# Kernel tuning notes

Measured on AMD Instinct MI355X. Metric: run time of the kernel, lower is better.

## Reference

```python
import jax, jax.numpy as jnp
import numpy as np

SIGMA_DATA = 16.0
ALPHA_BOND = 1.0
ALPHA_DNA = 5.0
ALPHA_RNA = 5.0
ALPHA_LIGAND = 10.0
B, N_TOK, APT = 2, 256, 8
N_ATOM = N_TOK * APT
EPS = 1e-12  # inside sqrt to keep grads finite on the zero diagonal


def _pdist(x):
    # x: [*, A, 3] -> [*, A, A]
    d = x[..., :, None, :] - x[..., None, :, :]
    return jnp.sqrt(jnp.sum(d * d, axis=-1) + EPS)


def _atom_onehot(token_mask, num_atoms_per_token, n_atom):
    # [*, A, T]: atom l belongs to token j iff cum[j-1] <= l < cum[j]
    cum = jnp.cumsum(num_atoms_per_token, axis=-1)
    start = cum - num_atoms_per_token
    l = jnp.arange(n_atom)
    oh = (l[:, None] >= start[..., None, :]) & (l[:, None] < cum[..., None, :])
    return oh.astype(jnp.float32) * token_mask[..., None, :]


def _tok_to_atom(onehot, feat):
    return jnp.einsum('...lj,...j->...l', onehot, feat)


def _weighted_rigid_align(x, x_gt, w, mask):
    # AF3 Algorithm 28 (Kabsch); output is detached in the original.
    denom = jnp.sum(mask, -1, keepdims=True)                      # [*,1]
    w_mean = jnp.sum(w * mask, -1, keepdims=True) / denom         # [*,1]
    wm = (w * mask)[..., None]                                    # [*,A,1]
    mu = (jnp.sum(x * wm, -2) / denom) / w_mean                   # [*,3]
    mu_gt = (jnp.sum(x_gt * wm, -2) / denom) / w_mean
    xc = x - mu[..., None, :]
    xgc = x_gt - mu_gt[..., None, :]
    H = jnp.einsum('...ai,...aj->...ij', xgc * wm, xc)            # [*,3,3]
    U, _, Vh = jnp.linalg.svd(H)
    det = jnp.linalg.det(U @ Vh)
    s = jnp.concatenate([jnp.ones(det.shape + (2,), H.dtype), jnp.sign(det)[..., None]], -1)
    R = U @ (Vh * s[..., :, None])                                # U @ diag(1,1,sign) @ Vh
    return jax.lax.stop_gradient(xc @ jnp.swapaxes(R, -1, -2) + mu_gt[..., None, :])


def _diffusion_loss(x, gt, gt_mask, is_p, is_d, is_r, is_l, tb, tm, npt, t):
    A = x.shape[-2]
    oh = _atom_onehot(tm, npt, A)                                 # [*,A,T]
    dx = _pdist(x)
    dx_gt = _pdist(gt)
    pair_mask = gt_mask[..., :, None] * gt_mask[..., None, :]

    # ---- bond loss (Eq. 5) ----
    is_poly = is_p + is_d + is_r
    bm_tok = tb * (is_poly[..., None, :] * is_l[..., None])       # [*,T,T]
    bm = jnp.einsum('...ij,...li->...lj', bm_tok, oh)
    bm = jnp.einsum('...lj,...mj->...lm', bm, oh)                 # [*,A,A]
    m = bm * pair_mask
    l_bond = jnp.sum((dx - dx_gt) ** 2 * m, (-1, -2)) / jnp.sum(m, (-1, -2))

    # ---- smooth LDDT (Alg. 27) ----
    d = jnp.abs(dx_gt - dx)
    e = 0.25 * (jax.nn.sigmoid(0.5 - d) + jax.nn.sigmoid(1.0 - d)
                + jax.nn.sigmoid(2.0 - d) + jax.nn.sigmoid(4.0 - d))
    is_nuc = _tok_to_atom(oh, is_d + is_r)                        # [*,A]
    c = ((dx_gt < 30).astype(x.dtype) * is_nuc[..., None]
         + (dx_gt < 15).astype(x.dtype) * (1.0 - is_nuc[..., None]))
    m2 = (1.0 - jnp.eye(A, dtype=x.dtype)) * pair_mask
    msum = jnp.sum(m2, (-1, -2))
    ce_mean = jnp.sum(c * e * m2, (-1, -2)) / msum
    c_mean = jnp.sum(c * m2, (-1, -2)) / msum
    l_lddt = 1.0 - ce_mean / c_mean

    # ---- weighted MSE (Eq. 3), gt aligned onto x ----
    w_tok = 1.0 + is_d * ALPHA_DNA + is_r * ALPHA_RNA + is_l * ALPHA_LIGAND
    w_atom = _tok_to_atom(oh, w_tok)                              # [*,A]
    sg = jax.lax.stop_gradient
    gt_al = _weighted_rigid_align(sg(gt), sg(x), sg(w_atom), sg(gt_mask))
    l_mse = (1.0 / 3.0) * jnp.sum(jnp.sum((x - gt_al) ** 2, -1) * w_atom * gt_mask, -1) \
            / jnp.sum(gt_mask, -1)

    w_t = (t ** 2 + SIGMA_DATA ** 2) / (t + SIGMA_DATA) ** 2
    return jnp.mean(w_t * (l_mse + ALPHA_BOND * l_bond) + l_lddt)


def setup_inputs() -> dict:
    key = jax.random.key(0)
    k = jax.random.split(key, 9)
    x = jax.random.normal(k[0], (B, N_ATOM, 3), jnp.float32) * 10.0
    gt = x + jax.random.normal(k[1], (B, N_ATOM, 3), jnp.float32)
    return {
        'x': x,
        'gt_atom_positions': gt,
        'gt_atom_mask': jnp.ones((B, N_ATOM), jnp.float32),
        'is_protein': jax.random.uniform(k[2], (B, N_TOK), jnp.float32),
        'is_dna': jax.random.uniform(k[3], (B, N_TOK), jnp.float32),
        'is_rna': jax.random.uniform(k[4], (B, N_TOK), jnp.float32),
        'is_ligand': jax.random.uniform(k[5], (B, N_TOK), jnp.float32),
        'token_bonds': jax.random.uniform(k[6], (B, N_TOK, N_TOK), jnp.float32),
        'token_mask': jnp.ones((B, N_TOK), jnp.float32),
        'num_atoms_per_token': jnp.full((B, N_TOK), APT, jnp.int32),
        't': jax.random.uniform(k[7], (B,), jnp.float32) * 10.0 + 0.1,
    }


def reference(x, gt_atom_positions, gt_atom_mask, is_protein, is_dna, is_rna,
              is_ligand, token_bonds, token_mask, num_atoms_per_token, t):
    return _diffusion_loss(x, gt_atom_positions, gt_atom_mask, is_protein, is_dna,
                           is_rna, is_ligand, token_bonds, token_mask,
                           num_atoms_per_token, t)
```

## Files before the change

kernel.cpp:

```cpp
#include <hip/hip_runtime.h>
#include <math.h>

#define BATCH 2
#define NTOK  256
#define NATOM 2048
#define TL 128
#define TM 64
#define NPB 512
#define TBBUF 1600

__device__ __forceinline__ float frcp(float x)  { return __builtin_amdgcn_rcpf(x); }
__device__ __forceinline__ float fsqrt_(float x){ return __builtin_amdgcn_sqrtf(x); }

__device__ __forceinline__ double wred64(double v) {
    for (int o = 32; o > 0; o >>= 1) v += __shfl_down(v, o, 64);
    return v;
}
__device__ __forceinline__ float fred64(float v) {
    for (int o = 32; o > 0; o >>= 1) v += __shfl_down(v, o, 64);
    return v;
}

__device__ void kabsch_from_sums(const double* sh, float* Rf, float* muf, double* masksum) {
    double wmsum = sh[1];
    double H[3][3];
    for (int i = 0; i < 3; i++)
        for (int j = 0; j < 3; j++)
            H[i][j] = sh[8 + i * 3 + j] - sh[2 + i] * sh[5 + j] / wmsum;
    double A[3][3];
    for (int j = 0; j < 3; j++) for (int k = 0; k < 3; k++) {
        double s = 0; for (int i = 0; i < 3; i++) s += H[i][j] * H[i][k];
        A[j][k] = s;
    }
    double V[3][3] = {{1, 0, 0}, {0, 1, 0}, {0, 0, 1}};
    for (int sweep = 0; sweep < 8; ++sweep) {
        double off = fabs(A[0][1]) + fabs(A[0][2]) + fabs(A[1][2]);
        double diag = fabs(A[0][0]) + fabs(A[1][1]) + fabs(A[2][2]);
        if (off < 1e-13 * (diag + 1e-300)) break;
        for (int pi = 0; pi < 3; ++pi) {
            int pp_ = (pi == 2) ? 1 : 0;
            int qq_ = (pi == 0) ? 1 : 2;
            double apq = A[pp_][qq_];
            if (fabs(apq) < 1e-300) continue;
            double theta = (A[qq_][qq_] - A[pp_][pp_]) / (2.0 * apq);
            double t_ = ((theta >= 0) ? 1.0 : -1.0) / (fabs(theta) + sqrt(theta * theta + 1.0));
            double c_ = 1.0 / sqrt(t_ * t_ + 1.0), sn = t_ * c_;
            for (int k = 0; k < 3; k++) { double akp = A[k][pp_], akq = A[k][qq_];
                A[k][pp_] = c_ * akp - sn * akq; A[k][qq_] = sn * akp + c_ * akq; }
            for (int k = 0; k < 3; k++) { double apk = A[pp_][k], aqk = A[qq_][k];
                A[pp_][k] = c_ * apk - sn * aqk; A[qq_][k] = sn * apk + c_ * aqk; }
            for (int k = 0; k < 3; k++) { double vkp = V[k][pp_], vkq = V[k][qq_];
                V[k][pp_] = c_ * vkp - sn * vkq; V[k][qq_] = sn * vkp + c_ * vkq; }
        }
    }
    double lam[3] = {A[0][0], A[1][1], A[2][2]};
    int idx[3] = {0, 1, 2};
    for (int i = 0; i < 2; i++) for (int j = i + 1; j < 3; j++)
        if (lam[idx[j]] > lam[idx[i]]) { int tsw = idx[i]; idx[i] = idx[j]; idx[j] = tsw; }
    double Vs[3][3], sv[3];
    for (int k = 0; k < 3; k++) {
        sv[k] = sqrt(fmax(lam[idx[k]], 0.0));
        for (int i = 0; i < 3; i++) Vs[i][k] = V[i][idx[k]];
    }
    double U[3][3] = {{1, 0, 0}, {0, 1, 0}, {0, 0, 1}};
    for (int k = 0; k < 3; k++) {
        if (sv[k] > 1e-12 * sv[0] + 1e-300) {
            for (int i = 0; i < 3; i++) {
                double s = 0; for (int j = 0; j < 3; j++) s += H[i][j] * Vs[j][k];
                U[i][k] = s / sv[k];
            }
        } else if (k == 2) {
            U[0][2] = U[1][0] * U[2][1] - U[2][0] * U[1][1];
            U[1][2] = U[2][0] * U[0][1] - U[0][0] * U[2][1];
            U[2][2] = U[0][0] * U[1][1] - U[1][0] * U[0][1];
        }
    }
    double R0[3][3];
    for (int i = 0; i < 3; i++) for (int j = 0; j < 3; j++) {
        double s = 0; for (int k = 0; k < 3; k++) s += U[i][k] * Vs[j][k];
        R0[i][j] = s;
    }
    double det = R0[0][0] * (R0[1][1] * R0[2][2] - R0[1][2] * R0[2][1])
               - R0[0][1] * (R0[1][0] * R0[2][2] - R0[1][2] * R0[2][0])
               + R0[0][2] * (R0[1][0] * R0[2][1] - R0[1][1] * R0[2][0]);
    double dk[3] = {1.0, 1.0, (det < 0.0) ? -1.0 : 1.0};
    for (int i = 0; i < 3; i++) for (int j = 0; j < 3; j++) {
        double s = 0; for (int k = 0; k < 3; k++) s += U[i][k] * dk[k] * Vs[j][k];
        Rf[i * 3 + j] = (float)s;
    }
    for (int i = 0; i < 3; i++) {
        muf[i]     = (float)(sh[2 + i] / wmsum);
        muf[3 + i] = (float)(sh[5 + i] / wmsum);
    }
    *masksum = sh[0];
}

struct PairSh {
    int    cum[NTOK];
    float  isl[NTOK], poly[NTOK], nuc[NTOK], tmk[NTOK];
    int    wsum[4];
    float4 lx[TL], lg[TL], mx[TM], mg[TM];
    float  lnuc[TL];
    int    ltok[TL], mtok[TM], lrow[TL], mrel[TM];
    float  tbuf[TBBUF];
    int    info[6];
    float  pred[4][4];
};
struct AlignSh {
    int    cum[NTOK];
    float  wt[NTOK];
    int    wsum[4];
    float  aw[NATOM];
    double dred[4][17];
    float  Rf[9], muf[6];
    double msum;
    double mred[4];
};

__global__ __launch_bounds__(256) void pair_align_kernel(
    const float* __restrict__ x, const float* __restrict__ gt,
    const float* __restrict__ gmask, const float* __restrict__ tb,
    const float* __restrict__ is_p, const float* __restrict__ is_d,
    const float* __restrict__ is_r, const float* __restrict__ is_l,
    const float* __restrict__ tok_mask, const int* __restrict__ npt,
    float4* __restrict__ partials4, float* __restrict__ lmse)
{
    __shared__ __align__(16) char smem[sizeof(PairSh) > sizeof(AlignSh) ? sizeof(PairSh) : sizeof(AlignSh)];
    int id = blockIdx.x;
    int tid = threadIdx.x;
    int lane = tid & 63, wv = tid >> 6;

    if (id < 2 * NPB) {
        PairSh* s = (PairSh*)smem;
        int b = id >> 9;
        int slot = id & (NPB - 1);
        int l0 = (slot & 15) * TL;
        int m0 = (slot >> 4) * TM;

        {
            int n = npt[b * NTOK + tid];
            int v = n;
            #pragma unroll
            for (int o = 1; o < 64; o <<= 1) {
                int u = __shfl_up(v, o, 64);
                if (lane >= o) v += u;
            }
            if (lane == 63) s->wsum[wv] = v;
            float pd = is_d[b * NTOK + tid], pr = is_r[b * NTOK + tid];
            float pp = is_p[b * NTOK + tid], pl = is_l[b * NTOK + tid];
            s->isl[tid]  = pl;
            s->poly[tid] = pp + pd + pr;
            s->nuc[tid]  = pd + pr;
            s->tmk[tid]  = tok_mask[b * NTOK + tid];
            __syncthreads();
            int pref = 0;
            for (int w = 0; w < wv; w++) pref += s->wsum[w];
            s->cum[tid] = v + pref;
        }
        __syncthreads();
        int total = s->cum[NTOK - 1];

        const float* Xb = x + (size_t)b * NATOM * 3;
        const float* Gb = gt + (size_t)b * NATOM * 3;
        const float* Mb = gmask + (size_t)b * NATOM;

        if (tid < TL) {
            int l = l0 + tid;
            int tok = 0; float oh = 0.0f;
            if (l < total) {
                int lo = 0, hi = NTOK - 1;
                while (lo < hi) { int mid = (lo + hi) >> 1; if (s->cum[mid] > l) hi = mid; else lo = mid + 1; }
                tok = lo; oh = s->tmk[tok];
            }
            float ml = Mb[l];
            s->lx[tid] = make_float4(Xb[l * 3], Xb[l * 3 + 1], Xb[l * 3 + 2], ml);
            s->lg[tid] = make_float4(Gb[l * 3], Gb[l * 3 + 1], Gb[l * 3 + 2], s->isl[tok] * oh * ml);
            s->lnuc[tid] = s->nuc[tok] * oh;
            s->ltok[tid] = tok;
        } else if (tid < TL + TM) {
            int i = tid - TL, m = m0 + i;
            int tok = 0; float oh = 0.0f;
            if (m < total) {
                int lo = 0, hi = NTOK - 1;
                while (lo < hi) { int mid = (lo + hi) >> 1; if (s->cum[mid] > m) hi = mid; else lo = mid + 1; }
                tok = lo; oh = s->tmk[tok];
            }
            float mm = Mb[m];
            s->mx[i] = make_float4(Xb[m * 3], Xb[m * 3 + 1], Xb[m * 3 + 2], mm);
            s->mg[i] = make_float4(Gb[m * 3], Gb[m * 3 + 1], Gb[m * 3 + 2], s->poly[tok] * oh * mm);
            s->mtok[i] = tok;
        }
        __syncthreads();
        if (tid == 0) {
            int tl0 = s->ltok[0], tl1 = s->ltok[TL - 1];
            int tm0 = s->mtok[0], tm1 = s->mtok[TM - 1];
            int spanL = tl1 - tl0 + 1, spanM = tm1 - tm0 + 1;
            int stride = spanM | 1;
            int fits = (spanL * stride <= TBBUF);
            s->info[0] = fits; s->info[1] = stride; s->info[2] = spanM;
            s->info[3] = tl0; s->info[4] = tm0; s->info[5] = spanL;
        }
        __syncthreads();
        int fits = s->info[0], stride = s->info[1], spanM = s->info[2];
        int tl0 = s->info[3], tm0 = s->info[4], spanL = s->info[5];
        if (tid < TL) {
            int tk = s->ltok[tid];
            s->lrow[tid] = fits ? min(max(tk - tl0, 0), spanL - 1) * stride : tk * NTOK;
        } else if (tid < TL + TM) {
            int tk = s->mtok[tid - TL];
            s->mrel[tid - TL] = fits ? min(max(tk - tm0, 0), spanM - 1) : tk;
        }
        const float* tbg = tb + (size_t)b * NTOK * NTOK;
        if (fits) {
            int cnt = spanL * stride;
            for (int i = tid; i < cnt; i += 256) {
                int r = i / stride, cc = i - r * stride;
                if (cc < spanM) s->tbuf[i] = tbg[(tl0 + r) * NTOK + tm0 + cc];
            }
        }
        __syncthreads();

        int lt = tid & 31, mg = tid >> 5;
        float4 lxv[4], lgv[4]; float lnu[4]; int lrw[4], gli[4];
        #pragma unroll
        for (int k = 0; k < 4; k++) {
            int li = lt + 32 * k;
            lxv[k] = s->lx[li]; lgv[k] = s->lg[li];
            lnu[k] = s->lnuc[li]; lrw[k] = s->lrow[li]; gli[k] = l0 + li;
        }
        float bnum = 0.f, bden = 0.f, ce = 0.f, cs = 0.f;
        const float k1 = 0.60653066f, k2 = 0.36787944f, k3 = 0.13533528f, k4 = 0.018315639f;

        auto body = [&](auto ldtb) {
            int mstart = mg * 8;
            #pragma unroll 2
            for (int j = 0; j < 8; j++) {
                int m = mstart + j;
                float4 mxv = s->mx[m], mgv = s->mg[m];
                int mrel = s->mrel[m];
                int gmi = m0 + m;
                #pragma unroll
                for (int k = 0; k < 4; k++) {
                    float dx0 = lxv[k].x - mxv.x, dx1 = lxv[k].y - mxv.y, dx2 = lxv[k].z - mxv.z;
                    float dg0 = lgv[k].x - mgv.x, dg1 = lgv[k].y - mgv.y, dg2 = lgv[k].z - mgv.z;
                    float dxv = fsqrt_(fmaf(dx2, dx2, fmaf(dx1, dx1, fmaf(dx0, dx0, 1e-12f))));
                    float dgv = fsqrt_(fmaf(dg2, dg2, fmaf(dg1, dg1, fmaf(dg0, dg0, 1e-12f))));
                    float diff = dxv - dgv;
                    float tbv = ldtb(lrw[k], mrel);
                    float bmv = tbv * (lgv[k].w * mgv.w);
                    bden += bmv;
                    bnum = fmaf(diff * diff, bmv, bnum);
                    float d = fabsf(diff);
                    float u = __expf(d);
                    float e1 = frcp(fmaf(u, k1, 1.0f));
                    float e2 = frcp(fmaf(u, k2, 1.0f));
                    float e3 = frcp(fmaf(u, k3, 1.0f));
                    float e4 = frcp(fmaf(u, k4, 1.0f));
                    float es = (e1 + e2) + (e3 + e4);
                    float pm = lxv[k].w * mxv.w;
                    float ccv = dgv < 30.0f ? (dgv < 15.0f ? 1.0f : lnu[k]) : 0.0f;
                    float pm2 = (gli[k] != gmi) ? pm : 0.0f;
                    float cm2 = ccv * pm2;
                    cs += cm2;
                    ce = fmaf(cm2 * 0.25f, es, ce);
                }
            }
        };
        if (fits) body([&](int r, int c) -> float { return s->tbuf[r + c]; });
        else      body([&](int r, int c) -> float { return tbg[r + c]; });

        float vals[4] = {bnum, bden, ce, cs};
        #pragma unroll
        for (int q = 0; q < 4; q++) {
            float v = fred64(vals[q]);
            if (lane == 0) s->pred[wv][q] = v;
        }
        __syncthreads();
        if (tid == 0) {
            float4 o;
            o.x = s->pred[0][0] + s->pred[1][0] + s->pred[2][0] + s->pred[3][0];
            o.y = s->pred[0][1] + s->pred[1][1] + s->pred[2][1] + s->pred[3][1];
            o.z = s->pred[0][2] + s->pred[1][2] + s->pred[2][2] + s->pred[3][2];
            o.w = s->pred[0][3] + s->pred[1][3] + s->pred[2][3] + s->pred[3][3];
            partials4[(size_t)b * NPB + slot] = o;
        }
    } else {
        AlignSh* s = (AlignSh*)smem;
        int b = id - 2 * NPB;

        {
            int n = npt[b * NTOK + tid];
            int v = n;
            #pragma unroll
            for (int o = 1; o < 64; o <<= 1) {
                int u = __shfl_up(v, o, 64);
                if (lane >= o) v += u;
            }
            if (lane == 63) s->wsum[wv] = v;
            float pd = is_d[b * NTOK + tid], pr = is_r[b * NTOK + tid];
            float pl = is_l[b * NTOK + tid];
            s->wt[tid] = (1.0f + 5.0f * pd + 5.0f * pr + 10.0f * pl) * tok_mask[b * NTOK + tid];
            __syncthreads();
            int pref = 0;
            for (int w = 0; w < wv; w++) pref += s->wsum[w];
            s->cum[tid] = v + pref;
        }
        __syncthreads();
        int total = s->cum[NTOK - 1];

        const float* X = x + (size_t)b * NATOM * 3;
        const float* G = gt + (size_t)b * NATOM * 3;
        const float* M = gmask + (size_t)b * NATOM;

        double p[17];
        #pragma unroll
        for (int q = 0; q < 17; q++) p[q] = 0.0;
        for (int a = tid; a < NATOM; a += 256) {
            float w = 0.0f;
            if (a < total) {
                int lo = 0, hi = NTOK - 1;
                while (lo < hi) { int mid = (lo + hi) >> 1; if (s->cum[mid] > a) hi = mid; else lo = mid + 1; }
                w = s->wt[lo];
            }
            s->aw[a] = w;
            double m = M[a], wm = (double)w * m;
            double x0 = X[a * 3], x1 = X[a * 3 + 1], x2 = X[a * 3 + 2];
            double g0 = G[a * 3], g1 = G[a * 3 + 1], g2 = G[a * 3 + 2];
            p[0] += m; p[1] += wm;
            p[2] += wm * x0; p[3] += wm * x1; p[4] += wm * x2;
            p[5] += wm * g0; p[6] += wm * g1; p[7] += wm * g2;
            p[8]  += wm * x0 * g0; p[9]  += wm * x0 * g1; p[10] += wm * x0 * g2;
            p[11] += wm * x1 * g0; p[12] += wm * x1 * g1; p[13] += wm * x1 * g2;
            p[14] += wm * x2 * g0; p[15] += wm * x2 * g1; p[16] += wm * x2 * g2;
        }
        #pragma unroll
        for (int q = 0; q < 17; q++) {
            double v = wred64(p[q]);
            if (lane == 0) s->dred[wv][q] = v;
        }
        __syncthreads();
        if (tid == 0) {
            double sh[17];
            for (int q = 0; q < 17; q++)
                sh[q] = s->dred[0][q] + s->dred[1][q] + s->dred[2][q] + s->dred[3][q];
            double ms;
            kabsch_from_sums(sh, s->Rf, s->muf, &ms);
            s->msum = ms;
        }
        __syncthreads();

        float R00 = s->Rf[0], R01 = s->Rf[1], R02 = s->Rf[2];
        float R10 = s->Rf[3], R11 = s->Rf[4], R12 = s->Rf[5];
        float R20 = s->Rf[6], R21 = s->Rf[7], R22 = s->Rf[8];
        float mux0 = s->muf[0], mux1 = s->muf[1], mux2 = s->muf[2];
        float mug0 = s->muf[3], mug1 = s->muf[4], mug2 = s->muf[5];
        double part = 0.0;
        for (int a = tid; a < NATOM; a += 256) {
            float w = s->aw[a], m = M[a];
            float gc0 = G[a * 3] - mug0, gc1 = G[a * 3 + 1] - mug1, gc2 = G[a * 3 + 2] - mug2;
            float al0 = R00 * gc0 + R01 * gc1 + R02 * gc2 + mux0;
            float al1 = R10 * gc0 + R11 * gc1 + R12 * gc2 + mux1;
            float al2 = R20 * gc0 + R21 * gc1 + R22 * gc2 + mux2;
            float r0 = X[a * 3] - al0, r1 = X[a * 3 + 1] - al1, r2 = X[a * 3 + 2] - al2;
            part += (double)(w * m * (r0 * r0 + r1 * r1 + r2 * r2));
        }
        {
            double v = wred64(part);
            if (lane == 0) s->mred[wv] = v;
        }
        __syncthreads();
        if (tid == 0)
            lmse[b] = (float)((s->mred[0] + s->mred[1] + s->mred[2] + s->mred[3]) / (3.0 * s->msum));
    }
}

__global__ __launch_bounds__(256) void final_kernel(
    const float4* __restrict__ partials4, const float* __restrict__ lmse,
    const float* __restrict__ t, float* __restrict__ out)
{
    int tid = threadIdx.x, lane = tid & 63, wv = tid >> 6;
    double pr[2][4] = {{0, 0, 0, 0}, {0, 0, 0, 0}};
    #pragma unroll
    for (int b = 0; b < BATCH; b++)
        for (int sI = tid; sI < NPB; sI += 256) {
            float4 v = partials4[(size_t)b * NPB + sI];
            pr[b][0] += v.x; pr[b][1] += v.y; pr[b][2] += v.z; pr[b][3] += v.w;
        }
    __shared__ double sred[4][8];
    #pragma unroll
    for (int b = 0; b < BATCH; b++)
        #pragma unroll
        for (int q = 0; q < 4; q++) {
            double v = wred64(pr[b][q]);
            if (lane == 0) sred[wv][b * 4 + q] = v;
        }
    __syncthreads();
    if (tid == 0) {
        double tot = 0.0;
        for (int b = 0; b < BATCH; b++) {
            double bn = 0, bd = 0, ce = 0, cs = 0;
            for (int w = 0; w < 4; w++) {
                bn += sred[w][b * 4 + 0]; bd += sred[w][b * 4 + 1];
                ce += sred[w][b * 4 + 2]; cs += sred[w][b * 4 + 3];
            }
            double l_bond = bn / bd;
            double l_lddt = 1.0 - ce / cs;
            double tt = t[b];
            double w_t = (tt * tt + 256.0) / ((tt + 16.0) * (tt + 16.0));
            tot += w_t * ((double)lmse[b] + l_bond) + l_lddt;
        }
        out[0] = (float)(tot / (double)BATCH);
    }
}

extern "C" void kernel_launch(void* const* d_in, const int* in_sizes, int n_in,
                              void* d_out, int out_size, void* d_ws, size_t ws_size,
                              hipStream_t stream) {
    const float* x     = (const float*)d_in[0];
    const float* gt    = (const float*)d_in[1];
    const float* gmask = (const float*)d_in[2];
    const float* is_p  = (const float*)d_in[3];
    const float* is_d  = (const float*)d_in[4];
    const float* is_r  = (const float*)d_in[5];
    const float* is_l  = (const float*)d_in[6];
    const float* tb    = (const float*)d_in[7];
    const float* tm    = (const float*)d_in[8];
    const int*   npt   = (const int*)d_in[9];
    const float* t     = (const float*)d_in[10];
    float* out = (float*)d_out;

    float4* partials4 = (float4*)d_ws;
    float*  lmse      = (float*)((char*)d_ws + (size_t)BATCH * NPB * sizeof(float4));

    pair_align_kernel<<<2 * NPB + BATCH, 256, 0, stream>>>(
        x, gt, gmask, tb, is_p, is_d, is_r, is_l, tm, npt, partials4, lmse);
    final_kernel<<<1, 256, 0, stream>>>(partials4, lmse, t, out);
}
```

Measured before the change: 105.8 us.

## Schedule align blocks first, fp32 Kabsch, scatter atom-token map instead of binary search

```diff
diff --git a/kernel.cpp b/kernel.cpp
--- a/kernel.cpp
+++ b/kernel.cpp
@@ -21,53 +21,55 @@
     return v;
 }
 
-__device__ void kabsch_from_sums(const double* sh, float* Rf, float* muf, double* masksum) {
-    double wmsum = sh[1];
-    double H[3][3];
+__device__ void kabsch_from_sums(const double* shd, float* Rf, float* muf, double* masksum) {
+    double wmsum = shd[1];
+    float H[3][3];
     for (int i = 0; i < 3; i++)
         for (int j = 0; j < 3; j++)
-            H[i][j] = sh[8 + i * 3 + j] - sh[2 + i] * sh[5 + j] / wmsum;
-    double A[3][3];
+            H[i][j] = (float)(shd[8 + i * 3 + j] - shd[2 + i] * shd[5 + j] / wmsum);
+    float A[3][3];
     for (int j = 0; j < 3; j++) for (int k = 0; k < 3; k++) {
-        double s = 0; for (int i = 0; i < 3; i++) s += H[i][j] * H[i][k];
+        float s = 0.f; for (int i = 0; i < 3; i++) s = fmaf(H[i][j], H[i][k], s);
         A[j][k] = s;
     }
-    double V[3][3] = {{1, 0, 0}, {0, 1, 0}, {0, 0, 1}};
-    for (int sweep = 0; sweep < 8; ++sweep) {
-        double off = fabs(A[0][1]) + fabs(A[0][2]) + fabs(A[1][2]);
-        double diag = fabs(A[0][0]) + fabs(A[1][1]) + fabs(A[2][2]);
-        if (off < 1e-13 * (diag + 1e-300)) break;
+    float V[3][3] = {{1, 0, 0}, {0, 1, 0}, {0, 0, 1}};
+    for (int sweep = 0; sweep < 6; ++sweep) {
+        float off = fabsf(A[0][1]) + fabsf(A[0][2]) + fabsf(A[1][2]);
+        float diag = fabsf(A[0][0]) + fabsf(A[1][1]) + fabsf(A[2][2]);
+        if (off < 1e-7f * diag) break;
         for (int pi = 0; pi < 3; ++pi) {
             int pp_ = (pi == 2) ? 1 : 0;
             int qq_ = (pi == 0) ? 1 : 2;
-            double apq = A[pp_][qq_];
-            if (fabs(apq) < 1e-300) continue;
-            double theta = (A[qq_][qq_] - A[pp_][pp_]) / (2.0 * apq);
-            double t_ = ((theta >= 0) ? 1.0 : -1.0) / (fabs(theta) + sqrt(theta * theta + 1.0));
-            double c_ = 1.0 / sqrt(t_ * t_ + 1.0), sn = t_ * c_;
-            for (int k = 0; k < 3; k++) { double akp = A[k][pp_], akq = A[k][qq_];
+            float apq = A[pp_][qq_];
+            float sc = fabsf(A[pp_][pp_]) + fabsf(A[qq_][qq_]);
+            if (fabsf(apq) <= 1e-9f * sc) continue;
+            float theta = (A[qq_][qq_] - A[pp_][pp_]) * 0.5f * frcp(apq);
+            float t_ = ((theta >= 0.f) ? 1.0f : -1.0f) * frcp(fabsf(theta) + fsqrt_(fmaf(theta, theta, 1.0f)));
+            float c_ = frcp(fsqrt_(fmaf(t_, t_, 1.0f))), sn = t_ * c_;
+            for (int k = 0; k < 3; k++) { float akp = A[k][pp_], akq = A[k][qq_];
                 A[k][pp_] = c_ * akp - sn * akq; A[k][qq_] = sn * akp + c_ * akq; }
-            for (int k = 0; k < 3; k++) { double apk = A[pp_][k], aqk = A[qq_][k];
+            for (int k = 0; k < 3; k++) { float apk = A[pp_][k], aqk = A[qq_][k];
                 A[pp_][k] = c_ * apk - sn * aqk; A[qq_][k] = sn * apk + c_ * aqk; }
-            for (int k = 0; k < 3; k++) { double vkp = V[k][pp_], vkq = V[k][qq_];
+            for (int k = 0; k < 3; k++) { float vkp = V[k][pp_], vkq = V[k][qq_];
                 V[k][pp_] = c_ * vkp - sn * vkq; V[k][qq_] = sn * vkp + c_ * vkq; }
         }
     }
-    double lam[3] = {A[0][0], A[1][1], A[2][2]};
+    float lam[3] = {A[0][0], A[1][1], A[2][2]};
     int idx[3] = {0, 1, 2};
     for (int i = 0; i < 2; i++) for (int j = i + 1; j < 3; j++)
         if (lam[idx[j]] > lam[idx[i]]) { int tsw = idx[i]; idx[i] = idx[j]; idx[j] = tsw; }
-    double Vs[3][3], sv[3];
+    float Vs[3][3], sv[3];
     for (int k = 0; k < 3; k++) {
-        sv[k] = sqrt(fmax(lam[idx[k]], 0.0));
+        sv[k] = fsqrt_(fmaxf(lam[idx[k]], 0.0f));
         for (int i = 0; i < 3; i++) Vs[i][k] = V[i][idx[k]];
     }
-    double U[3][3] = {{1, 0, 0}, {0, 1, 0}, {0, 0, 1}};
+    float U[3][3] = {{1, 0, 0}, {0, 1, 0}, {0, 0, 1}};
     for (int k = 0; k < 3; k++) {
-        if (sv[k] > 1e-12 * sv[0] + 1e-300) {
+        if (sv[k] > 1e-6f * sv[0] + 1e-30f) {
+            float inv = frcp(sv[k]);
             for (int i = 0; i < 3; i++) {
-                double s = 0; for (int j = 0; j < 3; j++) s += H[i][j] * Vs[j][k];
-                U[i][k] = s / sv[k];
+                float s = 0.f; for (int j = 0; j < 3; j++) s = fmaf(H[i][j], Vs[j][k], s);
+                U[i][k] = s * inv;
             }
         } else if (k == 2) {
             U[0][2] = U[1][0] * U[2][1] - U[2][0] * U[1][1];
@@ -75,30 +77,28 @@
             U[2][2] = U[0][0] * U[1][1] - U[1][0] * U[0][1];
         }
     }
-    double R0[3][3];
+    float R0[3][3];
     for (int i = 0; i < 3; i++) for (int j = 0; j < 3; j++) {
-        double s = 0; for (int k = 0; k < 3; k++) s += U[i][k] * Vs[j][k];
+        float s = 0.f; for (int k = 0; k < 3; k++) s = fmaf(U[i][k], Vs[j][k], s);
         R0[i][j] = s;
     }
-    double det = R0[0][0] * (R0[1][1] * R0[2][2] - R0[1][2] * R0[2][1])
-               - R0[0][1] * (R0[1][0] * R0[2][2] - R0[1][2] * R0[2][0])
-               + R0[0][2] * (R0[1][0] * R0[2][1] - R0[1][1] * R0[2][0]);
-    double dk[3] = {1.0, 1.0, (det < 0.0) ? -1.0 : 1.0};
-    for (int i = 0; i < 3; i++) for (int j = 0; j < 3; j++) {
-        double s = 0; for (int k = 0; k < 3; k++) s += U[i][k] * dk[k] * Vs[j][k];
-        Rf[i * 3 + j] = (float)s;
-    }
+    float det = R0[0][0] * (R0[1][1] * R0[2][2] - R0[1][2] * R0[2][1])
+              - R0[0][1] * (R0[1][0] * R0[2][2] - R0[1][2] * R0[2][0])
+              + R0[0][2] * (R0[1][0] * R0[2][1] - R0[1][1] * R0[2][0]);
+    float s2 = (det < 0.0f) ? -1.0f : 1.0f;
+    for (int i = 0; i < 3; i++) for (int j = 0; j < 3; j++)
+        Rf[i * 3 + j] = fmaf(U[i][0], Vs[j][0], fmaf(U[i][1], Vs[j][1], s2 * U[i][2] * Vs[j][2]));
     for (int i = 0; i < 3; i++) {
-        muf[i]     = (float)(sh[2 + i] / wmsum);
-        muf[3 + i] = (float)(sh[5 + i] / wmsum);
-    }
-    *masksum = sh[0];
+        muf[i]     = (float)(shd[2 + i] / wmsum);
+        muf[3 + i] = (float)(shd[5 + i] / wmsum);
+    }
+    *masksum = shd[0];
 }
 
 struct PairSh {
-    int    cum[NTOK];
     float  isl[NTOK], poly[NTOK], nuc[NTOK], tmk[NTOK];
     int    wsum[4];
+    unsigned short atokp1[NATOM];
     float4 lx[TL], lg[TL], mx[TM], mg[TM];
     float  lnuc[TL];
     int    ltok[TL], mtok[TM], lrow[TL], mrel[TM];
@@ -107,8 +107,6 @@
     float  pred[4][4];
 };
 struct AlignSh {
-    int    cum[NTOK];
-    float  wt[NTOK];
     int    wsum[4];
     float  aw[NATOM];
     double dred[4][17];
@@ -130,15 +128,16 @@
     int tid = threadIdx.x;
     int lane = tid & 63, wv = tid >> 6;
 
-    if (id < 2 * NPB) {
+    if (id >= BATCH) {
         PairSh* s = (PairSh*)smem;
-        int b = id >> 9;
-        int slot = id & (NPB - 1);
+        int pid = id - BATCH;
+        int b = pid >> 9;
+        int slot = pid & (NPB - 1);
         int l0 = (slot & 15) * TL;
         int m0 = (slot >> 4) * TM;
 
+        int n = npt[b * NTOK + tid];
         {
-            int n = npt[b * NTOK + tid];
             int v = n;
             #pragma unroll
             for (int o = 1; o < 64; o <<= 1) {
@@ -152,13 +151,17 @@
             s->poly[tid] = pp + pd + pr;
             s->nuc[tid]  = pd + pr;
             s->tmk[tid]  = tok_mask[b * NTOK + tid];
+            #pragma unroll
+            for (int i = 0; i < NATOM / NTOK; i++) s->atokp1[tid + i * NTOK] = 0;
             __syncthreads();
             int pref = 0;
             for (int w = 0; w < wv; w++) pref += s->wsum[w];
-            s->cum[tid] = v + pref;
-        }
-        __syncthreads();
-        int total = s->cum[NTOK - 1];
+            int cum = v + pref;
+            int end = min(cum, NATOM), start = min(cum - n, NATOM);
+            unsigned short tk1 = (unsigned short)(tid + 1);
+            for (int i = start; i < end; i++) s->atokp1[i] = tk1;
+        }
+        __syncthreads();
 
         const float* Xb = x + (size_t)b * NATOM * 3;
         const float* Gb = gt + (size_t)b * NATOM * 3;
@@ -166,12 +169,9 @@
 
         if (tid < TL) {
             int l = l0 + tid;
-            int tok = 0; float oh = 0.0f;
-            if (l < total) {
-                int lo = 0, hi = NTOK - 1;
-                while (lo < hi) { int mid = (lo + hi) >> 1; if (s->cum[mid] > l) hi = mid; else lo = mid + 1; }
-                tok = lo; oh = s->tmk[tok];
-            }
+            int v = s->atokp1[l];
+            int tok = v ? v - 1 : 0;
+            float oh = v ? s->tmk[tok] : 0.0f;
             float ml = Mb[l];
             s->lx[tid] = make_float4(Xb[l * 3], Xb[l * 3 + 1], Xb[l * 3 + 2], ml);
             s->lg[tid] = make_float4(Gb[l * 3], Gb[l * 3 + 1], Gb[l * 3 + 2], s->isl[tok] * oh * ml);
@@ -179,12 +179,9 @@
             s->ltok[tid] = tok;
         } else if (tid < TL + TM) {
             int i = tid - TL, m = m0 + i;
-            int tok = 0; float oh = 0.0f;
-            if (m < total) {
-                int lo = 0, hi = NTOK - 1;
-                while (lo < hi) { int mid = (lo + hi) >> 1; if (s->cum[mid] > m) hi = mid; else lo = mid + 1; }
-                tok = lo; oh = s->tmk[tok];
-            }
+            int v = s->atokp1[m];
+            int tok = v ? v - 1 : 0;
+            float oh = v ? s->tmk[tok] : 0.0f;
             float mm = Mb[m];
             s->mx[i] = make_float4(Xb[m * 3], Xb[m * 3 + 1], Xb[m * 3 + 2], mm);
             s->mg[i] = make_float4(Gb[m * 3], Gb[m * 3 + 1], Gb[m * 3 + 2], s->poly[tok] * oh * mm);
@@ -196,7 +193,7 @@
             int tm0 = s->mtok[0], tm1 = s->mtok[TM - 1];
             int spanL = tl1 - tl0 + 1, spanM = tm1 - tm0 + 1;
             int stride = spanM | 1;
-            int fits = (spanL * stride <= TBBUF);
+            int fits = (spanL >= 1) && (spanM >= 1) && (spanL * stride <= TBBUF);
             s->info[0] = fits; s->info[1] = stride; s->info[2] = spanM;
             s->info[3] = tl0; s->info[4] = tm0; s->info[5] = spanL;
         }
@@ -286,7 +283,7 @@
         }
     } else {
         AlignSh* s = (AlignSh*)smem;
-        int b = id - 2 * NPB;
+        int b = id;
 
         {
             int n = npt[b * NTOK + tid];
@@ -297,16 +294,19 @@
                 if (lane >= o) v += u;
             }
             if (lane == 63) s->wsum[wv] = v;
+            #pragma unroll
+            for (int i = 0; i < NATOM / NTOK; i++) s->aw[tid + i * NTOK] = 0.0f;
             float pd = is_d[b * NTOK + tid], pr = is_r[b * NTOK + tid];
             float pl = is_l[b * NTOK + tid];
-            s->wt[tid] = (1.0f + 5.0f * pd + 5.0f * pr + 10.0f * pl) * tok_mask[b * NTOK + tid];
+            float wtv = (1.0f + 5.0f * pd + 5.0f * pr + 10.0f * pl) * tok_mask[b * NTOK + tid];
             __syncthreads();
             int pref = 0;
             for (int w = 0; w < wv; w++) pref += s->wsum[w];
-            s->cum[tid] = v + pref;
-        }
-        __syncthreads();
-        int total = s->cum[NTOK - 1];
+            int cum = v + pref;
+            int end = min(cum, NATOM), start = min(cum - n, NATOM);
+            for (int i = start; i < end; i++) s->aw[i] = wtv;
+        }
+        __syncthreads();
 
         const float* X = x + (size_t)b * NATOM * 3;
         const float* G = gt + (size_t)b * NATOM * 3;
@@ -316,14 +316,7 @@
         #pragma unroll
         for (int q = 0; q < 17; q++) p[q] = 0.0;
         for (int a = tid; a < NATOM; a += 256) {
-            float w = 0.0f;
-            if (a < total) {
-                int lo = 0, hi = NTOK - 1;
-                while (lo < hi) { int mid = (lo + hi) >> 1; if (s->cum[mid] > a) hi = mid; else lo = mid + 1; }
-                w = s->wt[lo];
-            }
-            s->aw[a] = w;
-            double m = M[a], wm = (double)w * m;
+            double m = M[a], wm = (double)s->aw[a] * m;
             double x0 = X[a * 3], x1 = X[a * 3 + 1], x2 = X[a * 3 + 2];
             double g0 = G[a * 3], g1 = G[a * 3 + 1], g2 = G[a * 3 + 2];
             p[0] += m; p[1] += wm;
@@ -358,9 +351,9 @@
         for (int a = tid; a < NATOM; a += 256) {
             float w = s->aw[a], m = M[a];
             float gc0 = G[a * 3] - mug0, gc1 = G[a * 3 + 1] - mug1, gc2 = G[a * 3 + 2] - mug2;
-            float al0 = R00 * gc0 + R01 * gc1 + R02 * gc2 + mux0;
-            float al1 = R10 * gc0 + R11 * gc1 + R12 * gc2 + mux1;
-            float al2 = R20 * gc0 + R21 * gc1 + R22 * gc2 + mux2;
+            float al0 = fmaf(R00, gc0, fmaf(R01, gc1, fmaf(R02, gc2, mux0)));
+            float al1 = fmaf(R10, gc0, fmaf(R11, gc1, fmaf(R12, gc2, mux1)));
+            float al2 = fmaf(R20, gc0, fmaf(R21, gc1, fmaf(R22, gc2, mux2)));
             float r0 = X[a * 3] - al0, r1 = X[a * 3 + 1] - al1, r2 = X[a * 3 + 2] - al2;
             part += (double)(w * m * (r0 * r0 + r1 * r1 + r2 * r2));
         }
@@ -432,7 +425,7 @@
     float4* partials4 = (float4*)d_ws;
     float*  lmse      = (float*)((char*)d_ws + (size_t)BATCH * NPB * sizeof(float4));
 
-    pair_align_kernel<<<2 * NPB + BATCH, 256, 0, stream>>>(
+    pair_align_kernel<<<BATCH + 2 * NPB, 256, 0, stream>>>(
         x, gt, gmask, tb, is_p, is_d, is_r, is_l, tm, npt, partials4, lmse);
     final_kernel<<<1, 256, 0, stream>>>(partials4, lmse, t, out);
 }
```

After: 96.42 us. 8.9% less time.
